# Performance work log

Hardware: AMD Instinct MI355X
Metric: run time of the kernel (lower is better)

Reference implementation:

```python
import jax, jax.numpy as jnp
import numpy as np

B, T, E, H = 4, 2048, 1024, 16
HD = E // H
SCALING = HD ** -0.5


def setup_inputs() -> dict:
    key = jax.random.key(0)
    k1, k2, k3, k4 = jax.random.split(key, 4)
    x = jax.random.normal(k1, (B, T, E), dtype=jnp.float32)
    # key_padding_mask: 1 = ignore. Pad the tail of each sequence; length >= T//2
    lengths = jax.random.randint(k2, (B,), T // 2, T + 1)
    key_padding_mask = (jnp.arange(T)[None, :] >= lengths[:, None]).astype(jnp.int32)
    # attn_mask: causal (1 above the diagonal = ignore)
    attn_mask = jnp.triu(jnp.ones((T, T), dtype=jnp.int32), k=1)
    in_proj_weight = jax.random.normal(k3, (3 * E, E), dtype=jnp.float32) * 0.02
    in_proj_bias = jnp.zeros((3 * E,), dtype=jnp.float32)
    out_proj_weight = jax.random.normal(k4, (E, E), dtype=jnp.float32) * 0.02
    out_proj_bias = jnp.zeros((E,), dtype=jnp.float32)
    return {
        "x": x,
        "key_padding_mask": key_padding_mask,
        "attn_mask": attn_mask,
        "in_proj_weight": in_proj_weight,
        "in_proj_bias": in_proj_bias,
        "out_proj_weight": out_proj_weight,
        "out_proj_bias": out_proj_bias,
    }


def reference(x, key_padding_mask, attn_mask, in_proj_weight, in_proj_bias,
              out_proj_weight, out_proj_bias):
    b, t, e = x.shape
    # qkv_same path: single fused projection then chunk(3, dim=-1)
    qkv = x @ in_proj_weight.T + in_proj_bias  # (b, t, 3e)
    q, k, v = jnp.split(qkv, 3, axis=-1)
    q = q * SCALING
    # Faithful to torch: view(tgt_len, b*h, hd).transpose(0,1) on a batch-first
    # contiguous tensor (row-major reshape, interleaves batch and time).
    q = jnp.swapaxes(q.reshape(t, b * H, HD), 0, 1)  # (b*h, t, hd)
    k = jnp.swapaxes(k.reshape(t, b * H, HD), 0, 1)
    v = jnp.swapaxes(v.reshape(t, b * H, HD), 0, 1)
    scores = jnp.einsum('bqd,bkd->bqk', q, k)  # (b*h, t, t)
    scores = jnp.where(attn_mask[None].astype(bool), -jnp.inf, scores)
    scores = scores.reshape(b, H, t, t)
    scores = jnp.where(key_padding_mask[:, None, None, :].astype(bool), -jnp.inf, scores)
    scores = scores.reshape(b * H, t, t)
    probs = jax.nn.softmax(scores, axis=-1)
    attn = jnp.einsum('bqk,bkd->bqd', probs, v)  # (b*h, t, hd)
    attn = attn.reshape(b, t, e)  # faithful row-major view back
    out = attn @ out_proj_weight.T + out_proj_bias
    return out
```

## Files before the change

### kernel.cpp

```cpp
#include <hip/hip_runtime.h>
#include <hip/hip_bf16.h>
#include <math.h>

typedef __bf16 bf16;
typedef __attribute__((ext_vector_type(8))) __bf16 bf16x8;
typedef __attribute__((ext_vector_type(4))) __bf16 bf16x4;
typedef __attribute__((ext_vector_type(2))) __bf16 bf16x2;
typedef __attribute__((ext_vector_type(4))) float f32x4;
typedef __attribute__((ext_vector_type(16))) float f32x16;


typedef const __attribute__((address_space(1))) void* gas_ptr;
typedef __attribute__((address_space(3))) void* las_ptr;

__device__ __forceinline__ void gl_lds16(const void* g, void* s) {
    __builtin_amdgcn_global_load_lds((gas_ptr)g, (las_ptr)s, 16, 0, 0);
}

__device__ __forceinline__ uint32_t pk2(float a, float b) {
    bf16x2 t; t[0] = (bf16)a; t[1] = (bf16)b;
    return __builtin_bit_cast(uint32_t, t);
}

#if __has_builtin(__builtin_amdgcn_exp2f)
__device__ __forceinline__ float ex2(float x) { return __builtin_amdgcn_exp2f(x); }
#else
__device__ __forceinline__ float ex2(float x) { return exp2f(x); }
#endif

#define MFMA32(a, b, c) __builtin_amdgcn_mfma_f32_32x32x16_bf16(a, b, c, 0, 0, 0)
#define MFMA16(a, b, c) __builtin_amdgcn_mfma_f32_16x16x32_bf16(a, b, c, 0, 0, 0)

__global__ __launch_bounds__(256) void cvt_f32_bf16(const float* __restrict__ in,
                                                    bf16* __restrict__ out, int n) {
    int i = (blockIdx.x * 256 + threadIdx.x) * 4;
    if (i >= n) return;
    float4 v = *(const float4*)(in + i);
    bf16x4 o;
    o[0] = (bf16)v.x; o[1] = (bf16)v.y; o[2] = (bf16)v.z; o[3] = (bf16)v.w;
    *(bf16x4*)(out + i) = o;
}

__device__ __forceinline__ void gemm_core(const bf16* __restrict__ Abase,
                                          const bf16* __restrict__ Bbase,
                                          bf16 (&As)[2][4096], bf16 (&Bs)[2][4096],
                                          f32x4 (&acc)[4][4], int tid) {
    const int l = tid & 63;
    const int w = tid >> 6;
    const int wr = (w >> 1) * 64;
    const int wc = (w & 1) * 64;
    const int fr_row = l & 15;
    const int fr_col = 8 * (l >> 4);

#define STAGE(buf, k0)                                                        \
    {                                                                         \
        _Pragma("unroll")                                                     \
        for (int p = 0; p < 2; ++p) {                                         \
            const int ei = (p * 256 + tid) * 8;                               \
            const int row = ei >> 5;                                          \
            const int col = ei & 31;                                          \
            gl_lds16(Abase + row * 1024 + (k0) + col, (char*)As[buf] + ei * 2);\
            gl_lds16(Bbase + row * 1024 + (k0) + col, (char*)Bs[buf] + ei * 2);\
        }                                                                     \
    }

    STAGE(0, 0);
    __syncthreads();
    int cur = 0;
    for (int k0 = 0; k0 < 1024; k0 += 32) {
        if (k0 + 32 < 1024) STAGE(cur ^ 1, k0 + 32);
        bf16x8 af[4], bfr[4];
#pragma unroll
        for (int m = 0; m < 4; ++m)
            af[m] = *(const bf16x8*)&As[cur][(wr + m * 16 + fr_row) * 32 + fr_col];
#pragma unroll
        for (int n = 0; n < 4; ++n)
            bfr[n] = *(const bf16x8*)&Bs[cur][(wc + n * 16 + fr_row) * 32 + fr_col];
#pragma unroll
        for (int m = 0; m < 4; ++m)
#pragma unroll
            for (int n = 0; n < 4; ++n)
                acc[m][n] = MFMA16(af[m], bfr[n], acc[m][n]);
        __syncthreads();
        cur ^= 1;
    }
#undef STAGE
}

__global__ __launch_bounds__(256) void gemm_qkv(const bf16* __restrict__ A,
                                                const bf16* __restrict__ Bw,
                                                const float* __restrict__ bias,
                                                bf16* __restrict__ Qb,
                                                bf16* __restrict__ Kb,
                                                bf16* __restrict__ VTb) {
    __shared__ bf16 As[2][4096];
    __shared__ bf16 Bs[2][4096];
    const int tid = threadIdx.x;
    const int l = tid & 63;
    const int w = tid >> 6;
    const int bm0 = blockIdx.x * 128;
    const int bn0 = blockIdx.y * 128;
    f32x4 acc[4][4] = {};
    gemm_core(A + (size_t)bm0 * 1024, Bw + (size_t)bn0 * 1024, As, Bs, acc, tid);

    const int wr = (w >> 1) * 64;
    const int wc = (w & 1) * 64;
    const int rj = (l >> 4) * 4;
    const int cn = l & 15;
    const int sec = bn0 >> 10;
#pragma unroll
    for (int m = 0; m < 4; ++m) {
#pragma unroll
        for (int n = 0; n < 4; ++n) {
            const int gn = bn0 + wc + n * 16 + cn;
            const float bv = bias[gn];
            const int e = gn & 1023;
            const int eh = e >> 6;
            const int ed = e & 63;
#pragma unroll
            for (int j = 0; j < 4; ++j) {
                const int gm = bm0 + wr + m * 16 + rj + j;
                const float v = acc[m][n][j] + bv;
                const int bh = ((gm & 3) << 4) + eh;
                const int t = gm >> 2;
                if (sec == 0) {
                    Qb[bh * 131072 + t * 64 + ed] = (bf16)(v * 0.18033688f);
                } else if (sec == 1) {
                    Kb[bh * 131072 + t * 64 + ed] = (bf16)v;
                } else {
                    VTb[bh * 131072 + ed * 2048 + t] = (bf16)v;
                }
            }
        }
    }
}

__global__ __launch_bounds__(256) void gemm_out(const bf16* __restrict__ A,
                                                const bf16* __restrict__ Bw,
                                                const float* __restrict__ bias,
                                                float* __restrict__ Cout) {
    __shared__ bf16 As[2][4096];
    __shared__ bf16 Bs[2][4096];
    const int tid = threadIdx.x;
    const int l = tid & 63;
    const int w = tid >> 6;
    const int bm0 = blockIdx.x * 128;
    const int bn0 = blockIdx.y * 128;
    f32x4 acc[4][4] = {};
    gemm_core(A + (size_t)bm0 * 1024, Bw + (size_t)bn0 * 1024, As, Bs, acc, tid);

    const int wr = (w >> 1) * 64;
    const int wc = (w & 1) * 64;
    const int rj = (l >> 4) * 4;
    const int cn = l & 15;
#pragma unroll
    for (int m = 0; m < 4; ++m) {
#pragma unroll
        for (int n = 0; n < 4; ++n) {
            const int gn = bn0 + wc + n * 16 + cn;
            const float bv = bias[gn];
#pragma unroll
            for (int j = 0; j < 4; ++j) {
                const int gm = bm0 + wr + m * 16 + rj + j;
                Cout[(size_t)gm * 1024 + gn] = acc[m][n][j] + bv;
            }
        }
    }
}

__global__ __launch_bounds__(256) void attn_fwd5(const bf16* __restrict__ Qb,
                                                 const bf16* __restrict__ Kb,
                                                 const bf16* __restrict__ VTb,
                                                 const int* __restrict__ kpm,
                                                 bf16* __restrict__ Ob) {
    __shared__ __align__(16) char Ks[2][8192];
    __shared__ __align__(16) char Vs[2][8192];
    __shared__ int s_len;

    const int tid = threadIdx.x;
    const int l = tid & 63;
    const int w = tid >> 6;
    const int hi = l >> 5;
    const int l31 = l & 31;

    const int bid = blockIdx.x;
    const int j = bid >> 3;
    const int bh = (bid & 7) * 8 + (j & 7);
    const int p = 15 - (j >> 3);
    const int qt0 = p * 128;
    const int c = bh >> 4;

    if (tid == 0) s_len = 2048;
    __syncthreads();
    {
        const int base = c * 2048 + tid * 8;
        int4 a = *(const int4*)(kpm + base);
        int4 b = *(const int4*)(kpm + base + 4);
        int lm = 2048;
        if (b.w) lm = tid * 8 + 7;
        if (b.z) lm = tid * 8 + 6;
        if (b.y) lm = tid * 8 + 5;
        if (b.x) lm = tid * 8 + 4;
        if (a.w) lm = tid * 8 + 3;
        if (a.z) lm = tid * 8 + 2;
        if (a.y) lm = tid * 8 + 1;
        if (a.x) lm = tid * 8 + 0;
        if (lm < 2048) atomicMin(&s_len, lm);
    }
    __syncthreads();
    const int len = s_len;

    const int nt = min(2 * p + 2, (len + 63) >> 6);
    const int wt = min(2 * p + (w >> 1) + 1, nt);

    const int qg = qt0 + w * 32 + l31;
    bf16x8 qa[4];
    const bf16* Qrow = Qb + (size_t)bh * 131072 + (size_t)qg * 64 + hi * 8;
#pragma unroll
    for (int ks = 0; ks < 4; ++ks) qa[ks] = *(const bf16x8*)(Qrow + ks * 16);

    f32x16 o0 = {}, o1 = {};
    float mr = -1e30f, lr = 0.f;

    const char* Kg = (const char*)(Kb + (size_t)bh * 131072);
    const char* Vg = (const char*)(VTb + (size_t)bh * 131072);
    const int srow = tid >> 3;
    const int sbcol = (tid & 7) * 16;
    const int ldst = tid * 16;

#pragma unroll
    for (int g = 0; g < 2; ++g) {
        const int row = g * 32 + srow;
        const int scol = sbcol ^ ((row & 7) << 4);
        gl_lds16(Kg + row * 128 + scol, &Ks[0][g * 4096 + ldst]);
        gl_lds16(Vg + row * 4096 + scol, &Vs[0][g * 4096 + ldst]);
    }

    const int rbase = l31 * 128 + hi * 16;
    const int rxor = (l31 & 7) << 4;

    int cur = 0;
    for (int kt = 0; kt < nt; ++kt) {
        __syncthreads();
        if (kt + 1 < nt) {
            const int nk = (kt + 1) * 64;
#pragma unroll
            for (int g = 0; g < 2; ++g) {
                const int row = g * 32 + srow;
                const int scol = sbcol ^ ((row & 7) << 4);
                gl_lds16(Kg + (nk + row) * 128 + scol, &Ks[cur ^ 1][g * 4096 + ldst]);
                gl_lds16(Vg + row * 4096 + nk * 2 + scol, &Vs[cur ^ 1][g * 4096 + ldst]);
            }
        }
        if (kt < wt) {
            const int kt0 = kt * 64;
            f32x16 s0 = {}, s1 = {};
#pragma unroll
            for (int ks = 0; ks < 4; ++ks) {
                bf16x8 ka0 = *(const bf16x8*)&Ks[cur][(rbase + ks * 32) ^ rxor];
                bf16x8 ka1 = *(const bf16x8*)&Ks[cur][(4096 + rbase + ks * 32) ^ rxor];
                s0 = MFMA32(ka0, qa[ks], s0);
                s1 = MFMA32(ka1, qa[ks], s1);
            }
            const bool full = (kt0 + 63 <= qt0 + w * 32) && (kt0 + 64 <= len);
            if (!full) {
                const int kmax = min(qg, len - 1) - kt0;
#pragma unroll
                for (int r = 0; r < 16; ++r) {
                    const int kl = (r & 3) + 8 * (r >> 2) + 4 * hi;
                    if (kl > kmax) s0[r] = -1e30f;
                    if (kl + 32 > kmax) s1[r] = -1e30f;
                }
            }
            float mx = s0[0];
#pragma unroll
            for (int r = 1; r < 16; ++r) mx = fmaxf(mx, s0[r]);
#pragma unroll
            for (int r = 0; r < 16; ++r) mx = fmaxf(mx, s1[r]);
            mx = fmaxf(mx, __shfl_xor(mx, 32, 64));
            if (!__all(mx <= mr + 8.f)) {
                const float mn = fmaxf(mr, mx);
                const float al = ex2(mr - mn);
                lr *= al;
#pragma unroll
                for (int r = 0; r < 16; ++r) { o0[r] *= al; o1[r] *= al; }
                mr = mn;
            }
            float sum = 0.f;
#pragma unroll
            for (int r = 0; r < 16; ++r) { s0[r] = ex2(s0[r] - mr); sum += s0[r]; }
#pragma unroll
            for (int r = 0; r < 16; ++r) { s1[r] = ex2(s1[r] - mr); sum += s1[r]; }
            sum += __shfl_xor(sum, 32, 64);
            lr += sum;
            uint32_t pw[16];
#pragma unroll
            for (int u = 0; u < 4; ++u) {
#pragma unroll
                for (int h = 0; h < 2; ++h) {
                    pw[u * 2 + h] = pk2(s0[4 * u + 2 * h], s0[4 * u + 2 * h + 1]);
                    pw[8 + u * 2 + h] = pk2(s1[4 * u + 2 * h], s1[4 * u + 2 * h + 1]);
                }
            }
#pragma unroll
            for (int ks = 0; ks < 4; ++ks) {
                const int kk = ks >> 1;
                const int uA2 = (ks & 1) * 4;
                const uint32_t oA0 = pw[kk * 8 + uA2 + 0], oA1 = pw[kk * 8 + uA2 + 1];
                const uint32_t oB0 = pw[kk * 8 + uA2 + 2], oB1 = pw[kk * 8 + uA2 + 3];
                const uint32_t s0w = hi ? oA0 : oB0;
                const uint32_t s1w = hi ? oA1 : oB1;
                const uint32_t r0 = (uint32_t)__shfl_xor((int)s0w, 32, 64);
                const uint32_t r1 = (uint32_t)__shfl_xor((int)s1w, 32, 64);
                union { uint32_t u[4]; bf16x8 v; } pb;
                pb.u[0] = hi ? r0 : oA0;
                pb.u[1] = hi ? r1 : oA1;
                pb.u[2] = hi ? oB0 : r0;
                pb.u[3] = hi ? oB1 : r1;
                bf16x8 va0 = *(const bf16x8*)&Vs[cur][(rbase + ks * 32) ^ rxor];
                bf16x8 va1 = *(const bf16x8*)&Vs[cur][(4096 + rbase + ks * 32) ^ rxor];
                o0 = MFMA32(va0, pb.v, o0);
                o1 = MFMA32(va1, pb.v, o1);
            }
        }
        cur ^= 1;
    }
    const float inv = 1.f / lr;
    bf16* Orow = Ob + (size_t)bh * 131072 + (size_t)qg * 64;
#pragma unroll
    for (int r = 0; r < 16; ++r) {
        const int d = (r & 3) + 8 * (r >> 2) + 4 * hi;
        Orow[d] = (bf16)(o0[r] * inv);
        Orow[32 + d] = (bf16)(o1[r] * inv);
    }
}

extern "C" void kernel_launch(void* const* d_in, const int* in_sizes, int n_in,
                              void* d_out, int out_size, void* d_ws, size_t ws_size,
                              hipStream_t stream) {
    const float* x = (const float*)d_in[0];
    const int* kpm = (const int*)d_in[1];
    const float* wi = (const float*)d_in[3];
    const float* bi = (const float*)d_in[4];
    const float* wo = (const float*)d_in[5];
    const float* bo = (const float*)d_in[6];
    float* out = (float*)d_out;

    char* ws = (char*)d_ws;
    bf16* Qb  = (bf16*)(ws + (size_t)0);
    bf16* Kb  = (bf16*)(ws + ((size_t)16 << 20));
    bf16* VTb = (bf16*)(ws + ((size_t)32 << 20));
    bf16* xbf = (bf16*)(ws + ((size_t)48 << 20));
    bf16* Ob  = xbf;
    bf16* wib = (bf16*)(ws + ((size_t)64 << 20));
    bf16* wob = (bf16*)(ws + ((size_t)70 << 20));

    cvt_f32_bf16<<<8192, 256, 0, stream>>>(x, xbf, 8388608);
    cvt_f32_bf16<<<3072, 256, 0, stream>>>(wi, wib, 3145728);
    cvt_f32_bf16<<<1024, 256, 0, stream>>>(wo, wob, 1048576);

    gemm_qkv<<<dim3(64, 24), 256, 0, stream>>>(xbf, wib, bi, Qb, Kb, VTb);
    attn_fwd5<<<1024, 256, 0, stream>>>(Qb, Kb, VTb, kpm, Ob);
    gemm_out<<<dim3(64, 8), 256, 0, stream>>>(Ob, wob, bo, out);
}
```

Baseline: 183.4 us.

## Triple-buffer GEMM LDS staging with swizzled layout and vmcnt-based waits

The shared GEMM core moves from a double-buffered LDS pipeline to a three-stage ring, prefetching two k-tiles ahead. It uses explicit s_waitcnt vmcnt counts with a raw barrier instead of __syncthreads, so loads for the next tiles stay in flight during the MFMAs. It also XOR-swizzles the 16-byte column chunk by row to cut LDS bank conflicts on fragment reads. The cost is 50% more LDS per block, which may lower occupancy, and more fragile hand-written wait counts.

```diff
diff --git a/kernel.cpp b/kernel.cpp
--- a/kernel.cpp
+++ b/kernel.cpp
@@ -43,7 +43,7 @@
 
 __device__ __forceinline__ void gemm_core(const bf16* __restrict__ Abase,
                                           const bf16* __restrict__ Bbase,
-                                          bf16 (&As)[2][4096], bf16 (&Bs)[2][4096],
+                                          bf16 (&As)[3][4096], bf16 (&Bs)[3][4096],
                                           f32x4 (&acc)[4][4], int tid) {
     const int l = tid & 63;
     const int w = tid >> 6;
@@ -52,37 +52,49 @@
     const int fr_row = l & 15;
     const int fr_col = 8 * (l >> 4);
 
-#define STAGE(buf, k0)                                                        \
-    {                                                                         \
-        _Pragma("unroll")                                                     \
-        for (int p = 0; p < 2; ++p) {                                         \
-            const int ei = (p * 256 + tid) * 8;                               \
-            const int row = ei >> 5;                                          \
-            const int col = ei & 31;                                          \
+#define STAGE(buf, k0)                                                         \
+    {                                                                          \
+        _Pragma("unroll")                                                      \
+        for (int p = 0; p < 2; ++p) {                                          \
+            const int ei = (p * 256 + tid) * 8;                                \
+            const int row = ei >> 5;                                           \
+            const int col = (ei & 31) ^ ((row & 3) << 3);                      \
             gl_lds16(Abase + row * 1024 + (k0) + col, (char*)As[buf] + ei * 2);\
             gl_lds16(Bbase + row * 1024 + (k0) + col, (char*)Bs[buf] + ei * 2);\
-        }                                                                     \
+        }                                                                      \
     }
 
     STAGE(0, 0);
-    __syncthreads();
-    int cur = 0;
-    for (int k0 = 0; k0 < 1024; k0 += 32) {
-        if (k0 + 32 < 1024) STAGE(cur ^ 1, k0 + 32);
+    STAGE(1, 32);
+    asm volatile("s_waitcnt vmcnt(4)" ::: "memory");
+    __builtin_amdgcn_s_barrier();
+
+    int rd = 0;
+    for (int kt = 0; kt < 32; ++kt) {
+        if (kt < 30) {
+            const int st = rd >= 1 ? rd - 1 : rd + 2;
+            STAGE(st, (kt + 2) * 32);
+        }
         bf16x8 af[4], bfr[4];
 #pragma unroll
-        for (int m = 0; m < 4; ++m)
-            af[m] = *(const bf16x8*)&As[cur][(wr + m * 16 + fr_row) * 32 + fr_col];
-#pragma unroll
-        for (int n = 0; n < 4; ++n)
-            bfr[n] = *(const bf16x8*)&Bs[cur][(wc + n * 16 + fr_row) * 32 + fr_col];
+        for (int m = 0; m < 4; ++m) {
+            const int row = wr + m * 16 + fr_row;
+            af[m] = *(const bf16x8*)&As[rd][row * 32 + (fr_col ^ ((row & 3) << 3))];
+        }
+#pragma unroll
+        for (int n = 0; n < 4; ++n) {
+            const int row = wc + n * 16 + fr_row;
+            bfr[n] = *(const bf16x8*)&Bs[rd][row * 32 + (fr_col ^ ((row & 3) << 3))];
+        }
 #pragma unroll
         for (int m = 0; m < 4; ++m)
 #pragma unroll
             for (int n = 0; n < 4; ++n)
                 acc[m][n] = MFMA16(af[m], bfr[n], acc[m][n]);
-        __syncthreads();
-        cur ^= 1;
+        if (kt < 30) asm volatile("s_waitcnt vmcnt(4)" ::: "memory");
+        else         asm volatile("s_waitcnt vmcnt(0)" ::: "memory");
+        __builtin_amdgcn_s_barrier();
+        rd = rd < 2 ? rd + 1 : 0;
     }
 #undef STAGE
 }
@@ -93,8 +105,8 @@
                                                 bf16* __restrict__ Qb,
                                                 bf16* __restrict__ Kb,
                                                 bf16* __restrict__ VTb) {
-    __shared__ bf16 As[2][4096];
-    __shared__ bf16 Bs[2][4096];
+    __shared__ bf16 As[3][4096];
+    __shared__ bf16 Bs[3][4096];
     const int tid = threadIdx.x;
     const int l = tid & 63;
     const int w = tid >> 6;
@@ -139,8 +151,8 @@
                                                 const bf16* __restrict__ Bw,
                                                 const float* __restrict__ bias,
                                                 float* __restrict__ Cout) {
-    __shared__ bf16 As[2][4096];
-    __shared__ bf16 Bs[2][4096];
+    __shared__ bf16 As[3][4096];
+    __shared__ bf16 Bs[3][4096];
     const int tid = threadIdx.x;
     const int l = tid & 63;
     const int w = tid >> 6;
```

After: 191.4 us. 4.3% more time.
